# Optimization experiments

Hardware: AMD Instinct MI355X
Metric: run time of the kernel (lower is better)

Reference implementation:

```python
import jax, jax.numpy as jnp
import numpy as np

B, S = 256, 512
MEM, DK, DV, DS = 32, 128, 128, 256
NQ = 10000
ABILITY_SCALE = 3.0


def _kaiming(key, shape, fan_in):
    return jax.random.normal(key, shape, dtype=jnp.float32) * jnp.sqrt(2.0 / fan_in)


def setup_inputs() -> dict:
    key = jax.random.key(0)
    ks = jax.random.split(key, 20)
    q_data = jax.random.randint(ks[0], (B, S), 0, NQ + 1)
    qa_data = jax.random.randint(ks[1], (B, S), 0, 2 * NQ + 1)
    # embedding tables (padding_idx=0 row zeroed)
    q_table = _kaiming(ks[2], (NQ + 1, DK), DK).at[0].set(0.0)
    qa_table = _kaiming(ks[3], (2 * NQ + 1, DV), DV).at[0].set(0.0)
    # DKVMN memories
    key_memory = _kaiming(ks[4], (MEM, DK), DK)
    init_value_memory = _kaiming(ks[5], (MEM, DV), DV)
    # DKVMN write transforms (erase: sigmoid, add: tanh)
    W_erase = _kaiming(ks[6], (DV, DV), DV); b_erase = jnp.zeros((DV,), jnp.float32)
    W_add = _kaiming(ks[7], (DV, DV), DV); b_add = jnp.zeros((DV,), jnp.float32)
    # summary network: Linear(DV+DK -> DS) + tanh
    W_sum = _kaiming(ks[8], (DV + DK, DS), DV + DK); b_sum = jnp.zeros((DS,), jnp.float32)
    # student ability net: Linear(DS->DS)+tanh, Linear(DS->1)
    W_ab1 = _kaiming(ks[9], (DS, DS), DS); b_ab1 = jnp.zeros((DS,), jnp.float32)
    W_ab2 = _kaiming(ks[10], (DS, 1), DS); b_ab2 = jnp.zeros((1,), jnp.float32)
    # item difficulty net: Linear(DK->DK)+tanh, Linear(DK->1)
    W_df1 = _kaiming(ks[11], (DK, DK), DK); b_df1 = jnp.zeros((DK,), jnp.float32)
    W_df2 = _kaiming(ks[12], (DK, 1), DK); b_df2 = jnp.zeros((1,), jnp.float32)
    return dict(q_data=q_data, qa_data=qa_data, q_table=q_table, qa_table=qa_table,
                key_memory=key_memory, init_value_memory=init_value_memory,
                W_erase=W_erase, b_erase=b_erase, W_add=W_add, b_add=b_add,
                W_sum=W_sum, b_sum=b_sum, W_ab1=W_ab1, b_ab1=b_ab1,
                W_ab2=W_ab2, b_ab2=b_ab2, W_df1=W_df1, b_df1=b_df1,
                W_df2=W_df2, b_df2=b_df2)


def _forward(q_data, qa_data, q_table, qa_table, key_memory, init_value_memory,
             W_erase, b_erase, W_add, b_add, W_sum, b_sum,
             W_ab1, b_ab1, W_ab2, b_ab2, W_df1, b_df1, W_df2, b_df2):
    qe = q_table[q_data]            # [B,S,DK]
    qae = qa_table[qa_data]         # [B,S,DV]
    # attention weights for every timestep (depend only on q embeddings)
    w_all = jax.nn.softmax(jnp.einsum('bsd,md->bsm', qe, key_memory), axis=-1)  # [B,S,M]
    erase = jax.nn.sigmoid(qae @ W_erase + b_erase)   # [B,S,DV]
    add = jnp.tanh(qae @ W_add + b_add)               # [B,S,DV]
    Mv0 = jnp.broadcast_to(init_value_memory, (q_data.shape[0], MEM, DV))

    def step(Mv, xs):
        w, e, a = xs  # [B,M], [B,DV], [B,DV]
        read = jnp.einsum('bm,bmd->bd', w, Mv)  # read BEFORE write
        Mv = Mv * (1.0 - w[:, :, None] * e[:, None, :]) + w[:, :, None] * a[:, None, :]
        return Mv, read

    xs = (jnp.swapaxes(w_all, 0, 1), jnp.swapaxes(erase, 0, 1), jnp.swapaxes(add, 0, 1))
    _, reads = jax.lax.scan(step, Mv0, xs)          # reads: [S,B,DV]
    reads = jnp.swapaxes(reads, 0, 1)               # [B,S,DV]

    summary = jnp.tanh(jnp.concatenate([reads, qe], axis=-1) @ W_sum + b_sum)  # [B,S,DS]
    ability = jnp.tanh(summary @ W_ab1 + b_ab1) @ W_ab2 + b_ab2                # [B,S,1]
    difficulty = jnp.tanh(qe @ W_df1 + b_df1) @ W_df2 + b_df2                  # [B,S,1]
    z = ABILITY_SCALE * ability - difficulty
    pred = jax.nn.sigmoid(z)
    return (pred[..., 0], ability[..., 0], difficulty[..., 0], z[..., 0])


def reference(q_data, qa_data, q_table, qa_table, key_memory, init_value_memory,
              W_erase, b_erase, W_add, b_add, W_sum, b_sum,
              W_ab1, b_ab1, W_ab2, b_ab2, W_df1, b_df1, W_df2, b_df2):
    return _forward(q_data, qa_data, q_table, qa_table, key_memory, init_value_memory,
                    W_erase, b_erase, W_add, b_add, W_sum, b_sum,
                    W_ab1, b_ab1, W_ab2, b_ab2, W_df1, b_df1, W_df2, b_df2)
```

## Files before the change

### kernel.cpp

```cpp
#include <hip/hip_runtime.h>
#include <hip/hip_bf16.h>

typedef unsigned short u16;
typedef unsigned int   u32;

#define B_N   256
#define S_N   512
#define BSN   (B_N * S_N)
#define MEMN  32
#define DKN   128
#define DVN   128
#define DSN   256

typedef __attribute__((ext_vector_type(8))) short bf16x8;
typedef __attribute__((ext_vector_type(4))) float f32x4;

__device__ __forceinline__ float bf2f(u16 u) {
  union { u32 i; float f; } v; v.i = ((u32)u) << 16; return v.f;
}
__device__ __forceinline__ u16 f2bf(float f) {
  union { float f; u32 i; } v; v.f = f;
  u32 x = v.i;
  x += 0x7fffu + ((x >> 16) & 1u);
  return (u16)(x >> 16);
}
__device__ __forceinline__ u32 pack2(float a, float b) {
  return (u32)f2bf(a) | ((u32)f2bf(b) << 16);
}
__device__ __forceinline__ float sigmoid_fast(float x) { return 1.f / (1.f + __expf(-x)); }
__device__ __forceinline__ float tanh_fast(float x)    { return 1.f - 2.f / (__expf(2.f * x) + 1.f); }

#define GLOAD_LDS16(g, l)                                         \
  __builtin_amdgcn_global_load_lds(                               \
      (const __attribute__((address_space(1))) void*)(g),         \
      (__attribute__((address_space(3))) void*)(l), 16, 0, 0)

__global__ __launch_bounds__(256) void kPrep(
    const float* __restrict__ W_sum, const float* __restrict__ W_ab1,
    const float* __restrict__ W_er,  const float* __restrict__ W_ad,
    const float* __restrict__ key_mem, const float* __restrict__ W_df1,
    u16* __restrict__ WsumT, u16* __restrict__ Wab1T,
    u16* __restrict__ WerT,  u16* __restrict__ WaddT,
    u16* __restrict__ BqT)
{
  int e = blockIdx.x * 256 + threadIdx.x;
  if (e < 65536) {
    const int n = e >> 8, k = e & 255;
    WsumT[e] = f2bf(W_sum[k * 256 + n]);
  } else if (e < 131072) {
    e -= 65536;
    const int n = e >> 8, k = e & 255;
    Wab1T[e] = f2bf(W_ab1[k * 256 + n]);
  } else if (e < 147456) {
    e -= 131072;
    const int n = e >> 7, k = e & 127;
    WerT[e] = f2bf(W_er[k * 128 + n]);
  } else if (e < 163840) {
    e -= 147456;
    const int n = e >> 7, k = e & 127;
    WaddT[e] = f2bf(W_ad[k * 128 + n]);
  } else if (e < 184320) {
    e -= 163840;
    const int n = e >> 7, k = e & 127;
    BqT[e] = f2bf(n < 32 ? key_mem[n * 128 + k] : W_df1[k * 128 + (n - 32)]);
  }
}

__global__ __launch_bounds__(256) void kErAdd(
    const int* __restrict__ qa_data, const float* __restrict__ qa_table,
    const u16* __restrict__ WerT, const u16* __restrict__ WaddT,
    const float* __restrict__ b_er, const float* __restrict__ b_ad,
    u16* __restrict__ eras, u16* __restrict__ addb)
{
  __shared__ __align__(16) u16 As[4 * 128 * 32];
  __shared__ __align__(16) u16 Bs[2 * 128 * 32];
  const int tid = threadIdx.x;
  const int p0  = blockIdx.x * 128;
  const int sel = blockIdx.y;
  const u16*   Wt = sel ? WaddT : WerT;
  const float* bb = sel ? b_ad  : b_er;
  u16*       outp = sel ? addb  : eras;

  {
    const int r = tid >> 1, h = tid & 1;
    const long base = (long)qa_data[p0 + r] * DVN + h * 64;
    #pragma unroll
    for (int g = 0; g < 8; ++g) {
      const int k0 = h * 64 + g * 8;
      const float4 fa = *(const float4*)(qa_table + base + g * 8);
      const float4 fb = *(const float4*)(qa_table + base + g * 8 + 4);
      uint4 pk;
      pk.x = pack2(fa.x, fa.y); pk.y = pack2(fa.z, fa.w);
      pk.z = pack2(fb.x, fb.y); pk.w = pack2(fb.z, fb.w);
      *(uint4*)(As + (k0 >> 5) * 4096 + r * 32 + (k0 & 31)) = pk;
    }
  }
  {
    #pragma unroll
    for (int u = 0; u < 2; ++u) {
      const int f = tid + 256 * u;
      const int n = f >> 2, j = f & 3;
      *(uint4*)(Bs + n * 32 + j * 8) = *(const uint4*)(Wt + n * 128 + j * 8);
    }
  }
  __syncthreads();

  const int lane = tid & 63, wave = tid >> 6;
  const int wr = (wave >> 1) * 64, wc = (wave & 1) * 64;
  const int c15 = lane & 15, q = lane >> 4;

  f32x4 acc[4][4];
  #pragma unroll
  for (int b = 0; b < 4; ++b) {
    const float bv = bb[wc + 16 * b + c15];
    #pragma unroll
    for (int a = 0; a < 4; ++a) acc[a][b] = (f32x4){bv, bv, bv, bv};
  }

  for (int c = 0; c < 4; ++c) {
    const int cur = c & 1;
    uint4 st[2];
    const bool more = (c + 1 < 4);
    if (more) {
      #pragma unroll
      for (int u = 0; u < 2; ++u) {
        const int f = tid + 256 * u;
        const int n = f >> 2, j = f & 3;
        st[u] = *(const uint4*)(Wt + n * 128 + (c + 1) * 32 + j * 8);
      }
    }
    bf16x8 af[4], bf[4];
    #pragma unroll
    for (int a = 0; a < 4; ++a)
      af[a] = *(const bf16x8*)(As + c * 4096 + (wr + 16 * a + c15) * 32 + q * 8);
    #pragma unroll
    for (int b = 0; b < 4; ++b)
      bf[b] = *(const bf16x8*)(Bs + cur * 4096 + (wc + 16 * b + c15) * 32 + q * 8);
    #pragma unroll
    for (int a = 0; a < 4; ++a)
      #pragma unroll
      for (int b = 0; b < 4; ++b)
        acc[a][b] = __builtin_amdgcn_mfma_f32_16x16x32_bf16(af[a], bf[b], acc[a][b], 0, 0, 0);
    if (more) {
      #pragma unroll
      for (int u = 0; u < 2; ++u) {
        const int f = tid + 256 * u;
        const int n = f >> 2, j = f & 3;
        *(uint4*)(Bs + (cur ^ 1) * 4096 + n * 32 + j * 8) = st[u];
      }
    }
    __syncthreads();
  }

  const int colb = wc + c15;
  #pragma unroll
  for (int a = 0; a < 4; ++a) {
    #pragma unroll
    for (int r = 0; r < 4; ++r) {
      const int row = p0 + wr + 16 * a + 4 * q + r;
      u16* yp = outp + (long)row * DVN + colb;
      #pragma unroll
      for (int b = 0; b < 4; ++b) {
        const float v = sel ? tanh_fast(acc[a][b][r]) : sigmoid_fast(acc[a][b][r]);
        yp[16 * b] = f2bf(v);
      }
    }
  }
}

__global__ __launch_bounds__(256) void kSum(
    const u16* __restrict__ X, const u16* __restrict__ WsumT,
    const float* __restrict__ bias, u16* __restrict__ Y)
{
  __shared__ __align__(16) u16 As[8 * 128 * 32];
  __shared__ __align__(16) u16 Bs[2 * 128 * 32];
  const int tid = threadIdx.x;
  const int p0  = blockIdx.x * 128;
  const int j0  = blockIdx.y * 128;

  {
    #pragma unroll
    for (int u = 0; u < 16; ++u) {
      const int f = tid + 256 * u;
      const int r = f >> 5, j = f & 31;
      const uint4 raw = *(const uint4*)(X + (long)(p0 + r) * DSN + j * 8);
      *(uint4*)(As + (j >> 2) * 4096 + r * 32 + (j & 3) * 8) = raw;
    }
  }
  {
    #pragma unroll
    for (int u = 0; u < 2; ++u) {
      const int f = tid + 256 * u;
      const int n = f >> 2, j = f & 3;
      *(uint4*)(Bs + n * 32 + j * 8) = *(const uint4*)(WsumT + (j0 + n) * 256 + j * 8);
    }
  }
  __syncthreads();

  const int lane = tid & 63, wave = tid >> 6;
  const int wr = (wave >> 1) * 64, wc = (wave & 1) * 64;
  const int c15 = lane & 15, q = lane >> 4;

  f32x4 acc[4][4];
  #pragma unroll
  for (int b = 0; b < 4; ++b) {
    const float bv = bias[j0 + wc + 16 * b + c15];
    #pragma unroll
    for (int a = 0; a < 4; ++a) acc[a][b] = (f32x4){bv, bv, bv, bv};
  }

  for (int c = 0; c < 8; ++c) {
    const int cur = c & 1;
    uint4 st[2];
    const bool more = (c + 1 < 8);
    if (more) {
      #pragma unroll
      for (int u = 0; u < 2; ++u) {
        const int f = tid + 256 * u;
        const int n = f >> 2, j = f & 3;
        st[u] = *(const uint4*)(WsumT + (j0 + n) * 256 + (c + 1) * 32 + j * 8);
      }
    }
    bf16x8 af[4], bf[4];
    #pragma unroll
    for (int a = 0; a < 4; ++a)
      af[a] = *(const bf16x8*)(As + c * 4096 + (wr + 16 * a + c15) * 32 + q * 8);
    #pragma unroll
    for (int b = 0; b < 4; ++b)
      bf[b] = *(const bf16x8*)(Bs + cur * 4096 + (wc + 16 * b + c15) * 32 + q * 8);
    #pragma unroll
    for (int a = 0; a < 4; ++a)
      #pragma unroll
      for (int b = 0; b < 4; ++b)
        acc[a][b] = __builtin_amdgcn_mfma_f32_16x16x32_bf16(af[a], bf[b], acc[a][b], 0, 0, 0);
    if (more) {
      #pragma unroll
      for (int u = 0; u < 2; ++u) {
        const int f = tid + 256 * u;
        const int n = f >> 2, j = f & 3;
        *(uint4*)(Bs + (cur ^ 1) * 4096 + n * 32 + j * 8) = st[u];
      }
    }
    __syncthreads();
  }

  const int colb = j0 + wc + c15;
  #pragma unroll
  for (int a = 0; a < 4; ++a) {
    #pragma unroll
    for (int r = 0; r < 4; ++r) {
      const int row = p0 + wr + 16 * a + 4 * q + r;
      u16* yp = Y + (long)row * DSN + colb;
      #pragma unroll
      for (int b = 0; b < 4; ++b)
        yp[16 * b] = f2bf(tanh_fast(acc[a][b][r]));
    }
  }
}

__global__ __launch_bounds__(256) void kAb(
    const u16* __restrict__ X, const u16* __restrict__ Wab1T,
    const float* __restrict__ bias, const float* __restrict__ Wab2,
    float* __restrict__ part)
{
  __shared__ __align__(16) u16 As[8 * 128 * 32];
  __shared__ __align__(16) u16 Bs[2 * 128 * 32];
  const int tid = threadIdx.x;
  const int p0  = blockIdx.x * 128;
  const int j0  = blockIdx.y * 128;

  {
    #pragma unroll
    for (int u = 0; u < 16; ++u) {
      const int f = tid + 256 * u;
      const int r = f >> 5, j = f & 31;
      const uint4 raw = *(const uint4*)(X + (long)(p0 + r) * DSN + j * 8);
      *(uint4*)(As + (j >> 2) * 4096 + r * 32 + (j & 3) * 8) = raw;
    }
  }
  {
    #pragma unroll
    for (int u = 0; u < 2; ++u) {
      const int f = tid + 256 * u;
      const int n = f >> 2, j = f & 3;
      *(uint4*)(Bs + n * 32 + j * 8) = *(const uint4*)(Wab1T + (j0 + n) * 256 + j * 8);
    }
  }
  __syncthreads();

  const int lane = tid & 63, wave = tid >> 6;
  const int wr = (wave >> 1) * 64, wc = (wave & 1) * 64;
  const int c15 = lane & 15, q = lane >> 4;

  f32x4 acc[4][4];
  float w2v[4];
  #pragma unroll
  for (int b = 0; b < 4; ++b) {
    const int col = j0 + wc + 16 * b + c15;
    const float bv = bias[col];
    w2v[b] = Wab2[col];
    #pragma unroll
    for (int a = 0; a < 4; ++a) acc[a][b] = (f32x4){bv, bv, bv, bv};
  }

  for (int c = 0; c < 8; ++c) {
    const int cur = c & 1;
    uint4 st[2];
    const bool more = (c + 1 < 8);
    if (more) {
      #pragma unroll
      for (int u = 0; u < 2; ++u) {
        const int f = tid + 256 * u;
        const int n = f >> 2, j = f & 3;
        st[u] = *(const uint4*)(Wab1T + (j0 + n) * 256 + (c + 1) * 32 + j * 8);
      }
    }
    bf16x8 af[4], bf[4];
    #pragma unroll
    for (int a = 0; a < 4; ++a)
      af[a] = *(const bf16x8*)(As + c * 4096 + (wr + 16 * a + c15) * 32 + q * 8);
    #pragma unroll
    for (int b = 0; b < 4; ++b)
      bf[b] = *(const bf16x8*)(Bs + cur * 4096 + (wc + 16 * b + c15) * 32 + q * 8);
    #pragma unroll
    for (int a = 0; a < 4; ++a)
      #pragma unroll
      for (int b = 0; b < 4; ++b)
        acc[a][b] = __builtin_amdgcn_mfma_f32_16x16x32_bf16(af[a], bf[b], acc[a][b], 0, 0, 0);
    if (more) {
      #pragma unroll
      for (int u = 0; u < 2; ++u) {
        const int f = tid + 256 * u;
        const int n = f >> 2, j = f & 3;
        *(uint4*)(Bs + (cur ^ 1) * 4096 + n * 32 + j * 8) = st[u];
      }
    }
    __syncthreads();
  }

  float sv[4][4];
  #pragma unroll
  for (int a = 0; a < 4; ++a) {
    #pragma unroll
    for (int r = 0; r < 4; ++r) {
      float s = 0.f;
      #pragma unroll
      for (int b = 0; b < 4; ++b)
        s = fmaf(tanh_fast(acc[a][b][r]), w2v[b], s);
      s += __shfl_xor(s, 1, 64);
      s += __shfl_xor(s, 2, 64);
      s += __shfl_xor(s, 4, 64);
      s += __shfl_xor(s, 8, 64);
      sv[a][r] = s;
    }
  }
  float* red = (float*)Bs;
  if ((wave & 1) && c15 == 0) {
    #pragma unroll
    for (int a = 0; a < 4; ++a)
      #pragma unroll
      for (int r = 0; r < 4; ++r)
        red[wr + 16 * a + 4 * q + r] = sv[a][r];
  }
  __syncthreads();
  if (!(wave & 1) && c15 == 0) {
    #pragma unroll
    for (int a = 0; a < 4; ++a)
      #pragma unroll
      for (int r = 0; r < 4; ++r) {
        const int rr = wr + 16 * a + 4 * q + r;
        part[(long)blockIdx.y * BSN + p0 + rr] = sv[a][r] + red[rr];
      }
  }
}

__global__ __launch_bounds__(256) void kQe(
    const int* __restrict__ q_data, const float* __restrict__ q_table,
    const u16* __restrict__ BqT,
    const float* __restrict__ bdf1, const float* __restrict__ Wdf2,
    const float* __restrict__ bdf2,
    float* __restrict__ w_all, float* __restrict__ diff,
    u16* __restrict__ sin_buf)
{
  __shared__ __align__(16) u16 As[4 * 128 * 32];
  __shared__ __align__(16) u16 Bs[4 * 160 * 32];
  const int tid = threadIdx.x;
  const int p0  = blockIdx.x * 128;

  {
    const int r = tid >> 1, h = tid & 1;
    const long base = (long)q_data[p0 + r] * DKN + h * 64;
    #pragma unroll
    for (int g = 0; g < 8; ++g) {
      const int k0 = h * 64 + g * 8;
      const float4 fa = *(const float4*)(q_table + base + g * 8);
      const float4 fb = *(const float4*)(q_table + base + g * 8 + 4);
      uint4 pk;
      pk.x = pack2(fa.x, fa.y); pk.y = pack2(fa.z, fa.w);
      pk.z = pack2(fb.x, fb.y); pk.w = pack2(fb.z, fb.w);
      *(uint4*)(As + (k0 >> 5) * 4096 + r * 32 + (k0 & 31)) = pk;
      *(uint4*)(sin_buf + (long)(p0 + r) * DSN + DKN + k0) = pk;
    }
  }
  {
    #pragma unroll
    for (int u = 0; u < 10; ++u) {
      const int f = tid + 256 * u;
      const int n = f >> 4, jj = f & 15;
      *(uint4*)(Bs + (jj >> 2) * 5120 + n * 32 + (jj & 3) * 8) =
          *(const uint4*)(BqT + n * 128 + jj * 8);
    }
  }
  __syncthreads();

  const int lane = tid & 63, wave = tid >> 6;
  const int wr = (wave >> 1) * 64, wc = (wave & 1) * 80;
  const int c15 = lane & 15, q = lane >> 4;

  f32x4 acc[4][5];
  float w2v[5];
  #pragma unroll
  for (int b = 0; b < 5; ++b) {
    const int col = wc + 16 * b + c15;
    const float bv = (col < 32) ? 0.f : bdf1[col - 32];
    w2v[b] = (col < 32) ? 0.f : Wdf2[col - 32];
    #pragma unroll
    for (int a = 0; a < 4; ++a) acc[a][b] = (f32x4){bv, bv, bv, bv};
  }

  #pragma unroll
  for (int c = 0; c < 4; ++c) {
    bf16x8 af[4], bf[5];
    #pragma unroll
    for (int a = 0; a < 4; ++a)
      af[a] = *(const bf16x8*)(As + c * 4096 + (wr + 16 * a + c15) * 32 + q * 8);
    #pragma unroll
    for (int b = 0; b < 5; ++b)
      bf[b] = *(const bf16x8*)(Bs + c * 5120 + (wc + 16 * b + c15) * 32 + q * 8);
    #pragma unroll
    for (int a = 0; a < 4; ++a)
      #pragma unroll
      for (int b = 0; b < 5; ++b)
        acc[a][b] = __builtin_amdgcn_mfma_f32_16x16x32_bf16(af[a], bf[b], acc[a][b], 0, 0, 0);
  }

  if (wc == 0) {
    #pragma unroll
    for (int a = 0; a < 4; ++a) {
      #pragma unroll
      for (int r = 0; r < 4; ++r) {
        float s0 = acc[a][0][r], s1 = acc[a][1][r];
        float mx = fmaxf(s0, s1);
        mx = fmaxf(mx, __shfl_xor(mx, 1, 64));
        mx = fmaxf(mx, __shfl_xor(mx, 2, 64));
        mx = fmaxf(mx, __shfl_xor(mx, 4, 64));
        mx = fmaxf(mx, __shfl_xor(mx, 8, 64));
        const float e0 = __expf(s0 - mx), e1 = __expf(s1 - mx);
        float sm = e0 + e1;
        sm += __shfl_xor(sm, 1, 64);
        sm += __shfl_xor(sm, 2, 64);
        sm += __shfl_xor(sm, 4, 64);
        sm += __shfl_xor(sm, 8, 64);
        const float inv = 1.f / sm;
        const int row = p0 + wr + 16 * a + 4 * q + r;
        w_all[(long)row * MEMN + c15]      = e0 * inv;
        w_all[(long)row * MEMN + 16 + c15] = e1 * inv;
      }
    }
  }

  float sv[4][4];
  #pragma unroll
  for (int a = 0; a < 4; ++a) {
    #pragma unroll
    for (int r = 0; r < 4; ++r) {
      float s = 0.f;
      #pragma unroll
      for (int b = 0; b < 5; ++b)
        s = fmaf(tanh_fast(acc[a][b][r]), w2v[b], s);
      s += __shfl_xor(s, 1, 64);
      s += __shfl_xor(s, 2, 64);
      s += __shfl_xor(s, 4, 64);
      s += __shfl_xor(s, 8, 64);
      sv[a][r] = s;
    }
  }
  __syncthreads();
  float* red = (float*)As;
  if ((wave & 1) && c15 == 0) {
    #pragma unroll
    for (int a = 0; a < 4; ++a)
      #pragma unroll
      for (int r = 0; r < 4; ++r)
        red[wr + 16 * a + 4 * q + r] = sv[a][r];
  }
  __syncthreads();
  if (!(wave & 1) && c15 == 0) {
    const float bd = bdf2[0];
    #pragma unroll
    for (int a = 0; a < 4; ++a)
      #pragma unroll
      for (int r = 0; r < 4; ++r) {
        const int rr = wr + 16 * a + 4 * q + r;
        diff[p0 + rr] = sv[a][r] + red[rr] + bd;
      }
  }
}

#define CHUNK_BYTES 20480

#define KSTAGE(K, BUF)                                                        \
  {                                                                           \
    const char* wsrc = (const char*)(w_all + (pbase + (long)(K) * 32) * MEMN);\
    const char* esrc = (const char*)(eras + (pbase + (long)(K) * 32) * DVN);  \
    const char* asrc = (const char*)(addb + (pbase + (long)(K) * 32) * DVN);  \
    char* dst = lds + (BUF) * CHUNK_BYTES;                                    \
    _Pragma("unroll")                                                         \
    for (int r = 0; r < 5; ++r) {                                             \
      const int o = (tid + r * 256) * 16;                                     \
      const char* src = (o < 4096) ? (wsrc + o)                               \
                      : (o < 12288) ? (esrc + (o - 4096))                     \
                                    : (asrc + (o - 12288));                   \
      GLOAD_LDS16(src, dst + o);                                              \
    }                                                                         \
  }

__global__ __launch_bounds__(256) void kScan(
    const float* __restrict__ w_all, const u16* __restrict__ eras,
    const u16* __restrict__ addb, const float* __restrict__ init_mem,
    u16* __restrict__ sin_buf)
{
  __shared__ __align__(16) char lds[2 * CHUNK_BYTES + 512];
  const int tid = threadIdx.x;
  const int c = tid >> 1;
  const int h = tid & 1;
  const long pbase = (long)blockIdx.x * S_N;

  float Mv[16];
  #pragma unroll
  for (int m = 0; m < 16; ++m) Mv[m] = init_mem[(h * 16 + m) * DVN + c];

  u16* sp = sin_buf + pbase * DSN + c;

  KSTAGE(0, 0)
  for (int k = 0; k < 16; ++k) {
    __syncthreads();
    if (k + 1 < 16) KSTAGE(k + 1, (k + 1) & 1)

    const char*  wb  = lds + (k & 1) * CHUNK_BYTES;
    const f32x4* wl4 = (const f32x4*)wb;
    const u16*   el  = (const u16*)(wb + 4096);
    const u16*   al  = (const u16*)(wb + 12288);
    const int lb = k * 32;

    f32x4 Wr[3][4];
    u16 er[3], ar[3];
    #pragma unroll
    for (int i = 0; i < 4; ++i) Wr[0][i] = wl4[h * 4 + i];
    er[0] = el[c]; ar[0] = al[c];
    #pragma unroll
    for (int i = 0; i < 4; ++i) Wr[1][i] = wl4[8 + h * 4 + i];
    er[1] = el[128 + c]; ar[1] = al[128 + c];

    #pragma unroll
    for (int s = 0; s < 32; ++s) {
      const int cur = s % 3, nx2 = (s + 2) % 3;
      #pragma unroll
      for (int i = 0; i < 4; ++i) Wr[nx2][i] = wl4[(s + 2) * 8 + h * 4 + i];
      er[nx2] = el[(s + 2) * 128 + c];
      ar[nx2] = al[(s + 2) * 128 + c];
      {
        float ac0 = 0.f, ac1 = 0.f, ac2 = 0.f, ac3 = 0.f;
        #pragma unroll
        for (int i = 0; i < 4; ++i) {
          ac0 = fmaf(Wr[cur][i][0], Mv[4 * i + 0], ac0);
          ac1 = fmaf(Wr[cur][i][1], Mv[4 * i + 1], ac1);
          ac2 = fmaf(Wr[cur][i][2], Mv[4 * i + 2], ac2);
          ac3 = fmaf(Wr[cur][i][3], Mv[4 * i + 3], ac3);
        }
        float pr = (ac0 + ac1) + (ac2 + ac3);
        pr += __shfl_xor(pr, 1, 64);
        if (h == 0) sp[(long)(lb + s) * DSN] = f2bf(pr);
        const float ec = bf2f(er[cur]);
        const float an = -bf2f(ar[cur]);
        #pragma unroll
        for (int i = 0; i < 4; ++i) {
          #pragma unroll
          for (int j = 0; j < 4; ++j) {
            const float t = fmaf(ec, Mv[4 * i + j], an);
            Mv[4 * i + j] = fmaf(-Wr[cur][i][j], t, Mv[4 * i + j]);
          }
        }
      }
    }
  }
}

__global__ __launch_bounds__(256) void kOut(
    const float* __restrict__ part, const float* __restrict__ diff,
    const float* __restrict__ bab2, float* __restrict__ out)
{
  const int p = blockIdx.x * 256 + threadIdx.x;
  const float ab = part[p] + part[BSN + p] + bab2[0];
  const float d  = diff[p];
  const float z  = 3.0f * ab - d;
  out[p]           = sigmoid_fast(z);
  out[BSN + p]     = ab;
  out[2 * BSN + p] = d;
  out[3 * BSN + p] = z;
}

extern "C" void kernel_launch(void* const* d_in, const int* in_sizes, int n_in,
                              void* d_out, int out_size, void* d_ws, size_t ws_size,
                              hipStream_t stream)
{
  const int*   q_data   = (const int*)d_in[0];
  const int*   qa_data  = (const int*)d_in[1];
  const float* q_table  = (const float*)d_in[2];
  const float* qa_table = (const float*)d_in[3];
  const float* key_mem  = (const float*)d_in[4];
  const float* init_mem = (const float*)d_in[5];
  const float* W_erase  = (const float*)d_in[6];
  const float* b_erase  = (const float*)d_in[7];
  const float* W_add    = (const float*)d_in[8];
  const float* b_add    = (const float*)d_in[9];
  const float* W_sum    = (const float*)d_in[10];
  const float* b_sum    = (const float*)d_in[11];
  const float* W_ab1    = (const float*)d_in[12];
  const float* b_ab1    = (const float*)d_in[13];
  const float* W_ab2    = (const float*)d_in[14];
  const float* b_ab2    = (const float*)d_in[15];
  const float* W_df1    = (const float*)d_in[16];
  const float* b_df1    = (const float*)d_in[17];
  const float* W_df2    = (const float*)d_in[18];
  const float* b_df2    = (const float*)d_in[19];

  char* ws = (char*)d_ws;
  float* w_all = (float*)(ws + 0);
  u16*   eras  = (u16*)(ws + 16777216);
  u16*   addb  = (u16*)(ws + 50331648);
  u16*   sinb  = (u16*)(ws + 83886080);
  float* diffb = (float*)(ws + 150994944);
  float* part  = (float*)(ws + 151519232);
  u16*   WerT  = (u16*)(ws + 152567808);
  u16*   WaddT = (u16*)(ws + 152600576);
  u16*   WsumT = (u16*)(ws + 152633344);
  u16*   Wab1T = (u16*)(ws + 152764416);
  u16*   BqT   = (u16*)(ws + 152895488);
  u16*   summ  = eras;

  kPrep<<<dim3(720), 256, 0, stream>>>(W_sum, W_ab1, W_erase, W_add, key_mem, W_df1,
                                       WsumT, Wab1T, WerT, WaddT, BqT);
  kErAdd<<<dim3(BSN / 128, 2), 256, 0, stream>>>(qa_data, qa_table, WerT, WaddT,
                                                 b_erase, b_add, eras, addb);
  kQe<<<dim3(BSN / 128), 256, 0, stream>>>(q_data, q_table, BqT, b_df1, W_df2, b_df2,
                                           w_all, diffb, sinb);
  kScan<<<dim3(B_N), 256, 0, stream>>>(w_all, eras, addb, init_mem, sinb);
  kSum<<<dim3(BSN / 128, 2), 256, 0, stream>>>(sinb, WsumT, b_sum, summ);
  kAb<<<dim3(BSN / 128, 2), 256, 0, stream>>>(summ, Wab1T, b_ab1, W_ab2, part);
  kOut<<<dim3(BSN / 256), 256, 0, stream>>>(part, diffb, b_ab2, (float*)d_out);
}
```

Before: 379.2 us.

## Split scan value-memory columns across two blocks per batch element

The sequential memory scan now runs two blocks per batch element, each owning 64 of the 128 value columns. Within a block, four threads share a column and each holds 8 of the 32 memory slots, reduced with an extra cross-lane shuffle. This doubles the grid from 256 to 512 blocks to fill more of the GPU's compute units and halves the serial work per thread on the critical path. The cost is that each block restages the shared attention weights, and every step needs one more shuffle.

```diff
diff --git a/kernel.cpp b/kernel.cpp
--- a/kernel.cpp
+++ b/kernel.cpp
@@ -507,20 +507,29 @@
   }
 }
 
-#define CHUNK_BYTES 20480
+#define CHUNK_BYTES 12288
 
 #define KSTAGE(K, BUF)                                                        \
   {                                                                           \
     const char* wsrc = (const char*)(w_all + (pbase + (long)(K) * 32) * MEMN);\
-    const char* esrc = (const char*)(eras + (pbase + (long)(K) * 32) * DVN);  \
-    const char* asrc = (const char*)(addb + (pbase + (long)(K) * 32) * DVN);  \
+    const char* esrc = (const char*)(eras + (pbase + (long)(K) * 32) * DVN)   \
+                       + ch * 128;                                            \
+    const char* asrc = (const char*)(addb + (pbase + (long)(K) * 32) * DVN)   \
+                       + ch * 128;                                            \
     char* dst = lds + (BUF) * CHUNK_BYTES;                                    \
     _Pragma("unroll")                                                         \
-    for (int r = 0; r < 5; ++r) {                                             \
+    for (int r = 0; r < 3; ++r) {                                             \
       const int o = (tid + r * 256) * 16;                                     \
-      const char* src = (o < 4096) ? (wsrc + o)                               \
-                      : (o < 12288) ? (esrc + (o - 4096))                     \
-                                    : (asrc + (o - 12288));                   \
+      const char* src;                                                        \
+      if (o < 4096) {                                                         \
+        src = wsrc + o;                                                       \
+      } else if (o < 8192) {                                                  \
+        const int f = o - 4096;                                               \
+        src = esrc + (f >> 7) * 256 + (f & 127);                              \
+      } else {                                                                \
+        const int f = o - 8192;                                               \
+        src = asrc + (f >> 7) * 256 + (f & 127);                              \
+      }                                                                       \
       GLOAD_LDS16(src, dst + o);                                              \
     }                                                                         \
   }
@@ -532,15 +541,17 @@
 {
   __shared__ __align__(16) char lds[2 * CHUNK_BYTES + 512];
   const int tid = threadIdx.x;
-  const int c = tid >> 1;
-  const int h = tid & 1;
-  const long pbase = (long)blockIdx.x * S_N;
-
-  float Mv[16];
-  #pragma unroll
-  for (int m = 0; m < 16; ++m) Mv[m] = init_mem[(h * 16 + m) * DVN + c];
-
-  u16* sp = sin_buf + pbase * DSN + c;
+  const int ch  = blockIdx.x & 1;
+  const int lc  = tid >> 2;
+  const int gc  = ch * 64 + lc;
+  const int h   = tid & 3;
+  const long pbase = (long)(blockIdx.x >> 1) * S_N;
+
+  float Mv[8];
+  #pragma unroll
+  for (int m = 0; m < 8; ++m) Mv[m] = init_mem[(h * 8 + m) * DVN + gc];
+
+  u16* sp = sin_buf + pbase * DSN + gc;
 
   KSTAGE(0, 0)
   for (int k = 0; k < 16; ++k) {
@@ -550,29 +561,29 @@
     const char*  wb  = lds + (k & 1) * CHUNK_BYTES;
     const f32x4* wl4 = (const f32x4*)wb;
     const u16*   el  = (const u16*)(wb + 4096);
-    const u16*   al  = (const u16*)(wb + 12288);
+    const u16*   al  = (const u16*)(wb + 8192);
     const int lb = k * 32;
 
-    f32x4 Wr[3][4];
+    f32x4 Wr[3][2];
     u16 er[3], ar[3];
     #pragma unroll
-    for (int i = 0; i < 4; ++i) Wr[0][i] = wl4[h * 4 + i];
-    er[0] = el[c]; ar[0] = al[c];
-    #pragma unroll
-    for (int i = 0; i < 4; ++i) Wr[1][i] = wl4[8 + h * 4 + i];
-    er[1] = el[128 + c]; ar[1] = al[128 + c];
+    for (int i = 0; i < 2; ++i) Wr[0][i] = wl4[h * 2 + i];
+    er[0] = el[lc]; ar[0] = al[lc];
+    #pragma unroll
+    for (int i = 0; i < 2; ++i) Wr[1][i] = wl4[8 + h * 2 + i];
+    er[1] = el[64 + lc]; ar[1] = al[64 + lc];
 
     #pragma unroll
     for (int s = 0; s < 32; ++s) {
       const int cur = s % 3, nx2 = (s + 2) % 3;
-      #pragma unroll
-      for (int i = 0; i < 4; ++i) Wr[nx2][i] = wl4[(s + 2) * 8 + h * 4 + i];
-      er[nx2] = el[(s + 2) * 128 + c];
-      ar[nx2] = al[(s + 2) * 128 + c];
+      Wr[nx2][0] = wl4[(s + 2) * 8 + h * 2];
+      Wr[nx2][1] = wl4[(s + 2) * 8 + h * 2 + 1];
+      er[nx2] = el[(s + 2) * 64 + lc];
+      ar[nx2] = al[(s + 2) * 64 + lc];
       {
         float ac0 = 0.f, ac1 = 0.f, ac2 = 0.f, ac3 = 0.f;
         #pragma unroll
-        for (int i = 0; i < 4; ++i) {
+        for (int i = 0; i < 2; ++i) {
           ac0 = fmaf(Wr[cur][i][0], Mv[4 * i + 0], ac0);
           ac1 = fmaf(Wr[cur][i][1], Mv[4 * i + 1], ac1);
           ac2 = fmaf(Wr[cur][i][2], Mv[4 * i + 2], ac2);
@@ -580,11 +591,12 @@
         }
         float pr = (ac0 + ac1) + (ac2 + ac3);
         pr += __shfl_xor(pr, 1, 64);
+        pr += __shfl_xor(pr, 2, 64);
         if (h == 0) sp[(long)(lb + s) * DSN] = f2bf(pr);
         const float ec = bf2f(er[cur]);
         const float an = -bf2f(ar[cur]);
         #pragma unroll
-        for (int i = 0; i < 4; ++i) {
+        for (int i = 0; i < 2; ++i) {
           #pragma unroll
           for (int j = 0; j < 4; ++j) {
             const float t = fmaf(ec, Mv[4 * i + j], an);
@@ -655,7 +667,7 @@
                                                  b_erase, b_add, eras, addb);
   kQe<<<dim3(BSN / 128), 256, 0, stream>>>(q_data, q_table, BqT, b_df1, W_df2, b_df2,
                                            w_all, diffb, sinb);
-  kScan<<<dim3(B_N), 256, 0, stream>>>(w_all, eras, addb, init_mem, sinb);
+  kScan<<<dim3(B_N * 2), 256, 0, stream>>>(w_all, eras, addb, init_mem, sinb);
   kSum<<<dim3(BSN / 128, 2), 256, 0, stream>>>(sinb, WsumT, b_sum, summ);
   kAb<<<dim3(BSN / 128, 2), 256, 0, stream>>>(summ, Wab1T, b_ab1, W_ab2, part);
   kOut<<<dim3(BSN / 256), 256, 0, stream>>>(part, diffb, b_ab2, (float*)d_out);
```

Result: no change. 378.0 us (-0.3%).
